# Kernel optimization log

Measured on AMD Instinct MI355X. Metric: run time of the kernel, lower is better.

The kernel has to match this reference:

```python
import jax, jax.numpy as jnp
import numpy as np

EPS = 1e-5
NH, NP = 4, 4  # num_heads, num_points (num_levels = 1)


def layer_norm(x, g, b):
    m = jnp.mean(x, -1, keepdims=True)
    xc = x - m
    v = jnp.mean(xc * xc, -1, keepdims=True)
    return xc * jax.lax.rsqrt(v + EPS) * g + b


def setup_inputs() -> dict:
    key = jax.random.key(0)
    ks = jax.random.split(key, 8)
    B, C, H, W = 8, 256, 64, 64
    s = 0.02
    return {
        "x1": jax.random.normal(ks[0], (B, C, H, W), jnp.float32),
        "x2": jax.random.normal(ks[1], (B, C, H, W), jnp.float32),
        "ln1_g": jnp.ones((C,), jnp.float32),
        "ln1_b": jnp.zeros((C,), jnp.float32),
        "ln2_g": jnp.ones((C,), jnp.float32),
        "ln2_b": jnp.zeros((C,), jnp.float32),
        "pos_scale": jnp.ones((1,), jnp.float32),
        "W_off": jax.random.normal(ks[2], (C, NH * NP * 2), jnp.float32) * s,
        "b_off": jax.random.normal(ks[3], (NH * NP * 2,), jnp.float32) * 0.5,
        "W_att": jax.random.normal(ks[4], (C, NH * NP), jnp.float32) * s,
        "b_att": jnp.zeros((NH * NP,), jnp.float32),
        "W_val": jax.random.normal(ks[5], (C, C), jnp.float32) * s,
        "b_val": jnp.zeros((C,), jnp.float32),
        "W_out": jax.random.normal(ks[6], (C, C), jnp.float32) * s,
        "b_out": jnp.zeros((C,), jnp.float32),
    }


def reference(x1, x2, ln1_g, ln1_b, ln2_g, ln2_b, pos_scale,
              W_off, b_off, W_att, b_att, W_val, b_val, W_out, b_out):
    B, C, H, W = x1.shape
    Nq = H * W
    d = C // NH
    q_in = x1.reshape(B, C, Nq).transpose(0, 2, 1)   # (B, Nq, C)
    v_in = x2.reshape(B, C, Nq).transpose(0, 2, 1)   # (B, Nv, C), identity

    # ScaledSinuEmbedding positional encoding over the query sequence
    inv_freq = 1.0 / (10000.0 ** (jnp.arange(0, C, 2, dtype=jnp.float32) / C))
    sinu = jnp.arange(Nq, dtype=jnp.float32)[:, None] * inv_freq[None, :]
    qpos = jnp.concatenate([jnp.sin(sinu), jnp.cos(sinu)], -1) * pos_scale  # (Nq, C)

    query = layer_norm(q_in, ln1_g, ln1_b) + qpos[None]
    value = layer_norm(v_in, ln2_g, ln2_b) @ W_val + b_val                 # (B, Nv, C)
    value = value.reshape(B, Nq, NH, d).transpose(0, 2, 1, 3)              # (B, NH, Nv, d)

    off = (query @ W_off + b_off).reshape(B, Nq, NH, NP, 2)
    att = jax.nn.softmax((query @ W_att + b_att).reshape(B, Nq, NH, NP), axis=-1)

    # reference points: normalized pixel centers of the query grid
    ry, rx = jnp.meshgrid((jnp.arange(H, dtype=jnp.float32) + 0.5) / H,
                          (jnp.arange(W, dtype=jnp.float32) + 0.5) / W,
                          indexing="ij")
    ref = jnp.stack([rx.ravel(), ry.ravel()], -1)                          # (Nq, 2) as (x, y)

    norm = jnp.array([W, H], jnp.float32)  # offset_normalizer = (W, H)
    loc = ref[None, :, None, None, :] + off / norm                         # (B,Nq,NH,NP,2)
    loc = loc.transpose(0, 2, 1, 3, 4)                                     # (B,NH,Nq,NP,2)
    # grid_sample(align_corners=False): pixel = normalized * size - 0.5
    px = loc[..., 0] * W - 0.5
    py = loc[..., 1] * H - 0.5
    x0 = jnp.floor(px); y0 = jnp.floor(py)
    wx = px - x0; wy = py - y0
    x0i = x0.astype(jnp.int32); y0i = y0.astype(jnp.int32)

    def gather(ix, iy):
        # zero padding for out-of-bounds corners, like grid_sample(padding_mode='zeros')
        valid = ((ix >= 0) & (ix < W) & (iy >= 0) & (iy < H)).astype(value.dtype)
        idx = jnp.clip(iy, 0, H - 1) * W + jnp.clip(ix, 0, W - 1)          # (B,NH,Nq,NP)
        g = jnp.take_along_axis(value, idx.reshape(B, NH, Nq * NP, 1), axis=2)
        return g.reshape(B, NH, Nq, NP, d) * valid[..., None]

    sampled = (gather(x0i, y0i) * ((1 - wx) * (1 - wy))[..., None]
               + gather(x0i + 1, y0i) * (wx * (1 - wy))[..., None]
               + gather(x0i, y0i + 1) * ((1 - wx) * wy)[..., None]
               + gather(x0i + 1, y0i + 1) * (wx * wy)[..., None])          # (B,NH,Nq,NP,d)

    out = jnp.sum(sampled * att.transpose(0, 2, 1, 3)[..., None], axis=3)  # (B,NH,Nq,d)
    out = out.transpose(0, 2, 1, 3).reshape(B, Nq, C)
    out = out @ W_out + b_out + v_in                                       # + identity (x2)
    return out.transpose(0, 2, 1).reshape(B, C, H, W)
```

## Files before the change

kernel.cpp:

```cpp
#include <hip/hip_runtime.h>
#include <math.h>

namespace {
constexpr int kC = 256;
constexpr int kNq = 4096;
constexpr int kM = 32768;
}

typedef __attribute__((ext_vector_type(8))) short short8;
typedef __attribute__((ext_vector_type(4))) short short4v;
typedef __attribute__((ext_vector_type(4))) float f32x4;

__device__ inline unsigned short f2bf(float f) {
  union { float f; unsigned u; } v; v.f = f;
  unsigned r = (v.u + 0x7FFFu + ((v.u >> 16) & 1u)) >> 16;
  return (unsigned short)r;
}
__device__ inline float bf2f(unsigned short h) {
  union { unsigned u; float f; } v; v.u = ((unsigned)h) << 16; return v.f;
}
__device__ inline float uasf(unsigned u) {
  union { unsigned u; float f; } v; v.u = u; return v.f;
}

__global__ __launch_bounds__(256)
void prep_weights_kernel(const float* __restrict__ Wv, const float* __restrict__ Wo,
                         const float* __restrict__ Woff, const float* __restrict__ Watt,
                         const float* __restrict__ boff, const float* __restrict__ batt,
                         const float* __restrict__ ps,
                         unsigned short* __restrict__ WvT, unsigned short* __restrict__ WoT,
                         unsigned short* __restrict__ WoaT, float* __restrict__ QP) {
  __shared__ unsigned short Aq[64][264];
  const int blk = blockIdx.x;
  const int tid = threadIdx.x;
  const int i = blk * 256 + tid;
  {
    const int n = i >> 8, k = i & 255;
    WvT[i] = f2bf(Wv[k * 256 + n]);
    WoT[i] = f2bf(Wo[k * 256 + n]);
  }
  if (i < 16384) {
    const int j = i >> 8, k = i & 255;
    float v = 0.f;
    if (j < 32) v = Woff[k * 32 + j];
    else if (j < 48) v = Watt[k * 16 + (j - 32)];
    WoaT[i] = f2bf(v);
  }
  if (blk >= 64) return;

  const float scale = ps[0];
  const int i2 = (tid < 128) ? tid : (tid - 128);
  const float invf = powf(10000.f, -(float)(2 * i2) * (1.f / 256.f));
  for (int q = 0; q < 64; ++q) {
    const float a = (float)(blk * 64 + q) * invf;
    Aq[q][tid] = f2bf(((tid < 128) ? sinf(a) : cosf(a)) * scale);
  }
  __syncthreads();

  const int lane = tid & 63, w = tid >> 6;
  const int l15 = lane & 15, quad = lane >> 4;
  f32x4 acc[3];
#pragma unroll
  for (int j = 0; j < 3; ++j) acc[j] = (f32x4){0.f, 0.f, 0.f, 0.f};
#pragma unroll
  for (int s = 0; s < 8; ++s) {
    short8 af = *(const short8*)&Aq[w * 16 + l15][s * 32 + quad * 8];
    short8 wf[3];
#pragma unroll
    for (int t = 0; t < 3; ++t)
#pragma unroll
      for (int j = 0; j < 8; ++j) {
        const int k = s * 32 + quad * 8 + j;
        wf[t][j] = (short)f2bf((t < 2) ? Woff[k * 32 + t * 16 + l15]
                                       : Watt[k * 16 + l15]);
      }
#pragma unroll
    for (int j = 0; j < 3; ++j)
      acc[j] = __builtin_amdgcn_mfma_f32_16x16x32_bf16(af, wf[j], acc[j], 0, 0, 0);
  }
#pragma unroll
  for (int j = 0; j < 3; ++j) {
    const int n = j * 16 + l15;
    const float bn = (n < 32) ? boff[n] : batt[n - 32];
#pragma unroll
    for (int r = 0; r < 4; ++r) {
      const int q = blk * 64 + w * 16 + quad * 4 + r;
      QP[q * 48 + n] = acc[j][r] + bn;
    }
  }
}

__global__ __launch_bounds__(256)
void fused_ln_gemm_kernel(const float* __restrict__ x1, const float* __restrict__ x2,
                          const float* __restrict__ ln1_g, const float* __restrict__ ln1_b,
                          const float* __restrict__ ln2_g, const float* __restrict__ ln2_b,
                          const unsigned short* __restrict__ WvT,
                          const float* __restrict__ b_val, unsigned short* __restrict__ V,
                          const unsigned short* __restrict__ WoaT,
                          const float* __restrict__ QP, float* __restrict__ RAW) {
  __shared__ unsigned short As[64][264];
  __shared__ unsigned short sx[256][36];
  __shared__ float psum[2][32][4];
  __shared__ float smean[64];
  __shared__ float srstd[64];

  const int mode = blockIdx.x & 1;
  const int m0 = (blockIdx.x >> 1) * 64;
  const int b = m0 >> 12;
  const int n0 = m0 & 4095;
  const int tid = threadIdx.x;
  const int lane = tid & 63, w = tid >> 6;
  const float gc = mode ? ln1_g[tid] : ln2_g[tid];
  const float bc = mode ? ln1_b[tid] : ln2_b[tid];
  const float* Xb = (mode ? x1 : x2) + (size_t)b * kC * kNq;

  const int cbase = tid >> 3;
  const int q4 = (tid & 7) * 4;
  float4 v[16];
#pragma unroll
  for (int g = 0; g < 2; ++g)
#pragma unroll
    for (int it = 0; it < 8; ++it)
      v[g * 8 + it] = *(const float4*)&Xb[(size_t)(it * 32 + cbase) * kNq + n0 + g * 32 + q4];

  for (int g = 0; g < 2; ++g) {
    float s[4] = {0.f, 0.f, 0.f, 0.f}, sq[4] = {0.f, 0.f, 0.f, 0.f};
#pragma unroll
    for (int it = 0; it < 8; ++it) {
      const float4 f4 = v[g * 8 + it];
      const float e[4] = {f4.x, f4.y, f4.z, f4.w};
      short4v pk;
#pragma unroll
      for (int j = 0; j < 4; ++j) {
        s[j] += e[j];
        sq[j] += e[j] * e[j];
        pk[j] = (short)f2bf(e[j]);
      }
      *(short4v*)&sx[it * 32 + cbase][q4] = pk;
    }
#pragma unroll
    for (int d = 8; d <= 32; d <<= 1)
#pragma unroll
      for (int j = 0; j < 4; ++j) {
        s[j] += __shfl_xor(s[j], d);
        sq[j] += __shfl_xor(sq[j], d);
      }
    if (lane < 8) {
#pragma unroll
      for (int j = 0; j < 4; ++j) {
        psum[0][lane * 4 + j][w] = s[j];
        psum[1][lane * 4 + j][w] = sq[j];
      }
    }
    __syncthreads();
    if (tid < 32) {
      float S = 0.f, Q = 0.f;
#pragma unroll
      for (int ww = 0; ww < 4; ++ww) { S += psum[0][tid][ww]; Q += psum[1][tid][ww]; }
      const float m = S * (1.f / 256.f);
      const float var = Q * (1.f / 256.f) - m * m;
      smean[g * 32 + tid] = m;
      srstd[g * 32 + tid] = rsqrtf(var + 1e-5f);
    }
    __syncthreads();
#pragma unroll
    for (int k = 0; k < 8; ++k) {
      const short4v xs = *(const short4v*)&sx[tid][k * 4];
#pragma unroll
      for (int j = 0; j < 4; ++j) {
        const int row = g * 32 + k * 4 + j;
        As[row][tid] = f2bf((bf2f((unsigned short)xs[j]) - smean[row]) * srstd[row] * gc + bc);
      }
    }
    __syncthreads();
  }

  const int l15 = lane & 15, quad = lane >> 4;

  if (mode == 0) {
    f32x4 acc[4][4];
#pragma unroll
    for (int i = 0; i < 4; ++i)
#pragma unroll
      for (int j = 0; j < 4; ++j) acc[i][j] = (f32x4){0.f, 0.f, 0.f, 0.f};
#pragma unroll
    for (int s = 0; s < 8; ++s) {
      short8 af[4], wf[4];
#pragma unroll
      for (int t = 0; t < 4; ++t) af[t] = *(const short8*)&As[t * 16 + l15][s * 32 + quad * 8];
#pragma unroll
      for (int t = 0; t < 4; ++t)
        wf[t] = *(const short8*)&WvT[(size_t)(w * 64 + t * 16 + l15) * 256 + s * 32 + quad * 8];
#pragma unroll
      for (int i = 0; i < 4; ++i)
#pragma unroll
        for (int j = 0; j < 4; ++j)
          acc[i][j] = __builtin_amdgcn_mfma_f32_16x16x32_bf16(af[i], wf[j], acc[i][j], 0, 0, 0);
    }
#pragma unroll
    for (int i = 0; i < 4; ++i)
#pragma unroll
      for (int j = 0; j < 4; ++j) {
        const int n = w * 64 + j * 16 + l15;
        const float bn = b_val[n];
#pragma unroll
        for (int r = 0; r < 4; ++r) {
          const int m = m0 + i * 16 + quad * 4 + r;
          V[(size_t)m * 256 + n] = f2bf(acc[i][j][r] + bn);
        }
      }
  } else {
    f32x4 acc[3];
#pragma unroll
    for (int j = 0; j < 3; ++j) acc[j] = (f32x4){0.f, 0.f, 0.f, 0.f};
#pragma unroll
    for (int s = 0; s < 8; ++s) {
      short8 af = *(const short8*)&As[w * 16 + l15][s * 32 + quad * 8];
      short8 wf[3];
#pragma unroll
      for (int t = 0; t < 3; ++t)
        wf[t] = *(const short8*)&WoaT[(size_t)(t * 16 + l15) * 256 + s * 32 + quad * 8];
#pragma unroll
      for (int j = 0; j < 3; ++j)
        acc[j] = __builtin_amdgcn_mfma_f32_16x16x32_bf16(af, wf[j], acc[j], 0, 0, 0);
    }
#pragma unroll
    for (int j = 0; j < 3; ++j) {
      const int n = j * 16 + l15;
#pragma unroll
      for (int r = 0; r < 4; ++r) {
        const int m = m0 + w * 16 + quad * 4 + r;
        const int q = n0 + w * 16 + quad * 4 + r;
        RAW[(size_t)m * 48 + n] = acc[j][r] + QP[q * 48 + n];
      }
    }
  }
}

__global__ __launch_bounds__(256)
void sample_out_kernel(const float* __restrict__ RAW, const unsigned short* __restrict__ V,
                       const unsigned short* __restrict__ Wt,
                       const float* __restrict__ bias, const float* __restrict__ x2,
                       float* __restrict__ OUT) {
  __shared__ unsigned short Bs[64][264];
  __shared__ __align__(16) char smemA[32768];
  int (*sidx)[4] = (int(*)[4])smemA;
  float (*swgt)[4] = (float(*)[4])(smemA + 16384);
  float* ot = (float*)smemA;

  const int blk = blockIdx.x;
  const int b = blk & 7;
  const int tile = blk >> 3;
  const int m0 = b * 4096 + tile * 64;
  const int tid = threadIdx.x;

#pragma unroll
  for (int t = 0; t < 4; ++t) {
    const int trip = t * 256 + tid;
    const int q_l = trip >> 4, h = (trip >> 2) & 3, p = trip & 3;
    const int m = m0 + q_l;
    const float* raw = RAW + (size_t)m * 48;
    const float l0 = raw[32 + h * 4 + 0];
    const float l1 = raw[32 + h * 4 + 1];
    const float l2 = raw[32 + h * 4 + 2];
    const float l3 = raw[32 + h * 4 + 3];
    const float mx = fmaxf(fmaxf(l0, l1), fmaxf(l2, l3));
    const float e0 = expf(l0 - mx), e1 = expf(l1 - mx), e2 = expf(l2 - mx), e3 = expf(l3 - mx);
    const float lp = (p == 0) ? e0 : (p == 1) ? e1 : (p == 2) ? e2 : e3;
    const float attp = lp / (e0 + e1 + e2 + e3);

    const float ox = raw[h * 8 + p * 2 + 0];
    const float oy = raw[h * 8 + p * 2 + 1];
    const float px = (float)(m & 63) + ox;
    const float py = (float)((m >> 6) & 63) + oy;
    const float fx = floorf(px), fy = floorf(py);
    const float wx = px - fx, wy = py - fy;
    const int x0 = (int)fx, y0 = (int)fy;
#pragma unroll
    for (int c = 0; c < 4; ++c) {
      const int dx = c & 1, dy = c >> 1;
      const int xx = x0 + dx, yy = y0 + dy;
      const bool valid = (xx >= 0) & (xx < 64) & (yy >= 0) & (yy < 64);
      const float wc = (dx ? wx : 1.f - wx) * (dy ? wy : 1.f - wy) * attp;
      swgt[trip][c] = valid ? wc : 0.f;
      const int xc = min(max(xx, 0), 63), yc = min(max(yy, 0), 63);
      sidx[trip][c] = yc * 64 + xc;
    }
  }
  __syncthreads();

#pragma unroll
  for (int it = 0; it < 8; ++it) {
    const int lin = it * 256 + tid;
    const int q_l = lin >> 5, sub = lin & 31;
    const int h = sub >> 3, c8 = (sub & 7) * 8;
    const int trip0 = q_l * 16 + h * 4;
    const unsigned short* vb = V + (size_t)b * kNq * kC + h * 64 + c8;
    float acc[8] = {};
#pragma unroll
    for (int p = 0; p < 4; ++p) {
      const int4 idx = *(const int4*)&sidx[trip0 + p][0];
      const float4 wv = *(const float4*)&swgt[trip0 + p][0];
      const int ia[4] = {idx.x, idx.y, idx.z, idx.w};
      const float wa[4] = {wv.x, wv.y, wv.z, wv.w};
#pragma unroll
      for (int c = 0; c < 4; ++c) {
        const uint4 u = *(const uint4*)&vb[(size_t)ia[c] * kC];
        const float w = wa[c];
        acc[0] = fmaf(w, uasf(u.x << 16), acc[0]);
        acc[1] = fmaf(w, uasf(u.x & 0xffff0000u), acc[1]);
        acc[2] = fmaf(w, uasf(u.y << 16), acc[2]);
        acc[3] = fmaf(w, uasf(u.y & 0xffff0000u), acc[3]);
        acc[4] = fmaf(w, uasf(u.z << 16), acc[4]);
        acc[5] = fmaf(w, uasf(u.z & 0xffff0000u), acc[5]);
        acc[6] = fmaf(w, uasf(u.w << 16), acc[6]);
        acc[7] = fmaf(w, uasf(u.w & 0xffff0000u), acc[7]);
      }
    }
    short8 outv;
#pragma unroll
    for (int e = 0; e < 8; ++e) outv[e] = (short)f2bf(acc[e]);
    *(short8*)&Bs[q_l][h * 64 + c8] = outv;
  }
  __syncthreads();

  const int lane = tid & 63, w = tid >> 6;
  const int l15 = lane & 15, quad = lane >> 4;
  f32x4 acc[4][4];
#pragma unroll
  for (int i = 0; i < 4; ++i)
#pragma unroll
    for (int j = 0; j < 4; ++j) acc[i][j] = (f32x4){0.f, 0.f, 0.f, 0.f};
#pragma unroll
  for (int s = 0; s < 8; ++s) {
    short8 wf[4], bf[4];
#pragma unroll
    for (int t = 0; t < 4; ++t)
      wf[t] = *(const short8*)&Wt[(size_t)(w * 64 + t * 16 + l15) * 256 + s * 32 + quad * 8];
#pragma unroll
    for (int t = 0; t < 4; ++t) bf[t] = *(const short8*)&Bs[t * 16 + l15][s * 32 + quad * 8];
#pragma unroll
    for (int i = 0; i < 4; ++i)
#pragma unroll
      for (int j = 0; j < 4; ++j)
        acc[i][j] = __builtin_amdgcn_mfma_f32_16x16x32_bf16(wf[i], bf[j], acc[i][j], 0, 0, 0);
  }

  const int whalf = w >> 1;
  const int clbase = (w & 1) * 64;
  for (int ch = 0; ch < 2; ++ch) {
    __syncthreads();
    if (whalf == ch) {
#pragma unroll
      for (int i = 0; i < 4; ++i)
#pragma unroll
        for (int j = 0; j < 4; ++j)
#pragma unroll
          for (int r = 0; r < 4; ++r)
            ot[(clbase + i * 16 + quad * 4 + r) * 64 + j * 16 + l15] = acc[i][j][r];
    }
    __syncthreads();
#pragma unroll
    for (int t = 0; t < 8; ++t) {
      const int lin = t * 256 + tid;
      const int cl = lin >> 4, q4 = (lin & 15) * 4;
      const int c = ch * 128 + cl;
      const size_t rowbase = ((size_t)b * 256 + c) * 4096 + tile * 64;
      const float4 xv = *(const float4*)&x2[rowbase + q4];
      const float bc = bias[c];
      float4 o;
      o.x = ot[cl * 64 + q4 + 0] + bc + xv.x;
      o.y = ot[cl * 64 + q4 + 1] + bc + xv.y;
      o.z = ot[cl * 64 + q4 + 2] + bc + xv.z;
      o.w = ot[cl * 64 + q4 + 3] + bc + xv.w;
      *(float4*)&OUT[rowbase + q4] = o;
    }
  }
}

extern "C" void kernel_launch(void* const* d_in, const int* in_sizes, int n_in,
                              void* d_out, int out_size, void* d_ws, size_t ws_size,
                              hipStream_t stream) {
  const float* x1 = (const float*)d_in[0];
  const float* x2 = (const float*)d_in[1];
  const float* ln1_g = (const float*)d_in[2];
  const float* ln1_b = (const float*)d_in[3];
  const float* ln2_g = (const float*)d_in[4];
  const float* ln2_b = (const float*)d_in[5];
  const float* pos_scale = (const float*)d_in[6];
  const float* W_off = (const float*)d_in[7];
  const float* b_off = (const float*)d_in[8];
  const float* W_att = (const float*)d_in[9];
  const float* b_att = (const float*)d_in[10];
  const float* W_val = (const float*)d_in[11];
  const float* b_val = (const float*)d_in[12];
  const float* W_out = (const float*)d_in[13];
  const float* b_out = (const float*)d_in[14];
  float* out = (float*)d_out;

  char* ws = (char*)d_ws;
  const size_t plane2 = (size_t)kM * kC * sizeof(unsigned short);
  unsigned short* Vb   = (unsigned short*)(ws);
  float* RAW           = (float*)(ws + plane2);
  unsigned short* WvT  = (unsigned short*)(ws + plane2 + (size_t)kM * 48 * 4);
  unsigned short* WoT  = WvT + 65536;
  unsigned short* WoaT = WoT + 65536;
  float* QP            = (float*)(WoaT + 16384);

  prep_weights_kernel<<<256, 256, 0, stream>>>(W_val, W_out, W_off, W_att,
                                               b_off, b_att, pos_scale,
                                               WvT, WoT, WoaT, QP);
  fused_ln_gemm_kernel<<<1024, 256, 0, stream>>>(x1, x2, ln1_g, ln1_b, ln2_g, ln2_b,
                                                 WvT, b_val, Vb, WoaT, QP, RAW);
  sample_out_kernel<<<512, 256, 0, stream>>>(RAW, Vb, WoT, b_out, x2, out);
}
```

Baseline: 192.5 us.

## Restructure LN load mapping to drop staging buffer and spread positional prep

The fused LayerNorm+GEMM kernel now has each thread load 8 consecutive channels. It computes mean and variance for both 32-row groups in one pass and writes the normalized bf16 rows straight into the GEMM tile. This removes the bf16 staging buffer sx, two barriers per group, and a bf16 round-trip of x, and raises occupancy through launch bounds. The positional-encoding projection in prep_weights is spread over all blocks at 16 queries each, using angle-addition recurrences instead of per-element sin/cos. The recurrence can accumulate small rounding drift, and the new global load pattern is less coalesced per channel row.

```diff
diff --git a/kernel.cpp b/kernel.cpp
--- a/kernel.cpp
+++ b/kernel.cpp
@@ -15,9 +15,6 @@
   union { float f; unsigned u; } v; v.f = f;
   unsigned r = (v.u + 0x7FFFu + ((v.u >> 16) & 1u)) >> 16;
   return (unsigned short)r;
-}
-__device__ inline float bf2f(unsigned short h) {
-  union { unsigned u; float f; } v; v.u = ((unsigned)h) << 16; return v.f;
 }
 __device__ inline float uasf(unsigned u) {
   union { unsigned u; float f; } v; v.u = u; return v.f;
@@ -30,7 +27,7 @@
                          const float* __restrict__ ps,
                          unsigned short* __restrict__ WvT, unsigned short* __restrict__ WoT,
                          unsigned short* __restrict__ WoaT, float* __restrict__ QP) {
-  __shared__ unsigned short Aq[64][264];
+  __shared__ unsigned short Aq[16][264];
   const int blk = blockIdx.x;
   const int tid = threadIdx.x;
   const int i = blk * 256 + tid;
@@ -46,51 +43,50 @@
     else if (j < 48) v = Watt[k * 16 + (j - 32)];
     WoaT[i] = f2bf(v);
   }
-  if (blk >= 64) return;
 
   const float scale = ps[0];
   const int i2 = (tid < 128) ? tid : (tid - 128);
   const float invf = powf(10000.f, -(float)(2 * i2) * (1.f / 256.f));
-  for (int q = 0; q < 64; ++q) {
-    const float a = (float)(blk * 64 + q) * invf;
-    Aq[q][tid] = f2bf(((tid < 128) ? sinf(a) : cosf(a)) * scale);
+  const int q0 = blk * 16;
+  const float a0 = (float)q0 * invf;
+  float sv = sinf(a0), cv = cosf(a0);
+  const float sd = sinf(invf), cd = cosf(invf);
+#pragma unroll
+  for (int q = 0; q < 16; ++q) {
+    Aq[q][tid] = f2bf(((tid < 128) ? sv : cv) * scale);
+    const float ns = sv * cd + cv * sd;
+    const float nc = cv * cd - sv * sd;
+    sv = ns; cv = nc;
   }
   __syncthreads();
 
   const int lane = tid & 63, w = tid >> 6;
   const int l15 = lane & 15, quad = lane >> 4;
-  f32x4 acc[3];
-#pragma unroll
-  for (int j = 0; j < 3; ++j) acc[j] = (f32x4){0.f, 0.f, 0.f, 0.f};
-#pragma unroll
-  for (int s = 0; s < 8; ++s) {
-    short8 af = *(const short8*)&Aq[w * 16 + l15][s * 32 + quad * 8];
-    short8 wf[3];
-#pragma unroll
-    for (int t = 0; t < 3; ++t)
+  if (w < 3) {
+    f32x4 acc = (f32x4){0.f, 0.f, 0.f, 0.f};
+#pragma unroll
+    for (int s = 0; s < 8; ++s) {
+      const short8 af = *(const short8*)&Aq[l15][s * 32 + quad * 8];
+      short8 wf;
 #pragma unroll
       for (int j = 0; j < 8; ++j) {
         const int k = s * 32 + quad * 8 + j;
-        wf[t][j] = (short)f2bf((t < 2) ? Woff[k * 32 + t * 16 + l15]
-                                       : Watt[k * 16 + l15]);
-      }
-#pragma unroll
-    for (int j = 0; j < 3; ++j)
-      acc[j] = __builtin_amdgcn_mfma_f32_16x16x32_bf16(af, wf[j], acc[j], 0, 0, 0);
-  }
-#pragma unroll
-  for (int j = 0; j < 3; ++j) {
-    const int n = j * 16 + l15;
+        wf[j] = (short)f2bf((w < 2) ? Woff[k * 32 + w * 16 + l15]
+                                    : Watt[k * 16 + l15]);
+      }
+      acc = __builtin_amdgcn_mfma_f32_16x16x32_bf16(af, wf, acc, 0, 0, 0);
+    }
+    const int n = w * 16 + l15;
     const float bn = (n < 32) ? boff[n] : batt[n - 32];
 #pragma unroll
     for (int r = 0; r < 4; ++r) {
-      const int q = blk * 64 + w * 16 + quad * 4 + r;
-      QP[q * 48 + n] = acc[j][r] + bn;
-    }
-  }
-}
-
-__global__ __launch_bounds__(256)
+      const int q = q0 + quad * 4 + r;
+      QP[q * 48 + n] = acc[r] + bn;
+    }
+  }
+}
+
+__global__ __launch_bounds__(256, 4)
 void fused_ln_gemm_kernel(const float* __restrict__ x1, const float* __restrict__ x2,
                           const float* __restrict__ ln1_g, const float* __restrict__ ln1_b,
                           const float* __restrict__ ln2_g, const float* __restrict__ ln2_b,
@@ -99,8 +95,8 @@
                           const unsigned short* __restrict__ WoaT,
                           const float* __restrict__ QP, float* __restrict__ RAW) {
   __shared__ unsigned short As[64][264];
-  __shared__ unsigned short sx[256][36];
   __shared__ float psum[2][32][4];
+  __shared__ float psq[2][32][4];
   __shared__ float smean[64];
   __shared__ float srstd[64];
 
@@ -110,70 +106,91 @@
   const int n0 = m0 & 4095;
   const int tid = threadIdx.x;
   const int lane = tid & 63, w = tid >> 6;
-  const float gc = mode ? ln1_g[tid] : ln2_g[tid];
-  const float bc = mode ? ln1_b[tid] : ln2_b[tid];
+  const int l7 = tid & 7;
+  const int q4 = l7 * 4;
+  const int cb8 = (tid >> 3) * 8;
   const float* Xb = (mode ? x1 : x2) + (size_t)b * kC * kNq;
-
-  const int cbase = tid >> 3;
-  const int q4 = (tid & 7) * 4;
+  const float* gptr = mode ? ln1_g : ln2_g;
+  const float* bptr = mode ? ln1_b : ln2_b;
+
+  float4 gm[2], bv[2];
+  gm[0] = *(const float4*)&gptr[cb8];
+  gm[1] = *(const float4*)&gptr[cb8 + 4];
+  bv[0] = *(const float4*)&bptr[cb8];
+  bv[1] = *(const float4*)&bptr[cb8 + 4];
+
   float4 v[16];
 #pragma unroll
   for (int g = 0; g < 2; ++g)
 #pragma unroll
     for (int it = 0; it < 8; ++it)
-      v[g * 8 + it] = *(const float4*)&Xb[(size_t)(it * 32 + cbase) * kNq + n0 + g * 32 + q4];
-
+      v[g * 8 + it] = *(const float4*)&Xb[(size_t)(cb8 + it) * kNq + n0 + g * 32 + q4];
+
+  float s[2][4] = {}, sq[2][4] = {};
+#pragma unroll
+  for (int g = 0; g < 2; ++g)
+#pragma unroll
+    for (int it = 0; it < 8; ++it) {
+      const float* e = (const float*)&v[g * 8 + it];
+#pragma unroll
+      for (int j = 0; j < 4; ++j) {
+        s[g][j] += e[j];
+        sq[g][j] += e[j] * e[j];
+      }
+    }
+#pragma unroll
+  for (int d = 8; d <= 32; d <<= 1)
+#pragma unroll
+    for (int g = 0; g < 2; ++g)
+#pragma unroll
+      for (int j = 0; j < 4; ++j) {
+        s[g][j] += __shfl_xor(s[g][j], d);
+        sq[g][j] += __shfl_xor(sq[g][j], d);
+      }
+  if (lane < 8) {
+#pragma unroll
+    for (int g = 0; g < 2; ++g)
+#pragma unroll
+      for (int j = 0; j < 4; ++j) {
+        psum[g][q4 + j][w] = s[g][j];
+        psq[g][q4 + j][w] = sq[g][j];
+      }
+  }
+  __syncthreads();
+  if (tid < 64) {
+    const int g = tid >> 5, qq = tid & 31;
+    float S = 0.f, Q = 0.f;
+#pragma unroll
+    for (int ww = 0; ww < 4; ++ww) { S += psum[g][qq][ww]; Q += psq[g][qq][ww]; }
+    const float m = S * (1.f / 256.f);
+    const float var = Q * (1.f / 256.f) - m * m;
+    smean[tid] = m;
+    srstd[tid] = rsqrtf(var + 1e-5f);
+  }
+  __syncthreads();
+
+#pragma unroll
   for (int g = 0; g < 2; ++g) {
-    float s[4] = {0.f, 0.f, 0.f, 0.f}, sq[4] = {0.f, 0.f, 0.f, 0.f};
-#pragma unroll
-    for (int it = 0; it < 8; ++it) {
-      const float4 f4 = v[g * 8 + it];
-      const float e[4] = {f4.x, f4.y, f4.z, f4.w};
-      short4v pk;
-#pragma unroll
-      for (int j = 0; j < 4; ++j) {
-        s[j] += e[j];
-        sq[j] += e[j] * e[j];
-        pk[j] = (short)f2bf(e[j]);
-      }
-      *(short4v*)&sx[it * 32 + cbase][q4] = pk;
-    }
-#pragma unroll
-    for (int d = 8; d <= 32; d <<= 1)
-#pragma unroll
-      for (int j = 0; j < 4; ++j) {
-        s[j] += __shfl_xor(s[j], d);
-        sq[j] += __shfl_xor(sq[j], d);
-      }
-    if (lane < 8) {
-#pragma unroll
-      for (int j = 0; j < 4; ++j) {
-        psum[0][lane * 4 + j][w] = s[j];
-        psum[1][lane * 4 + j][w] = sq[j];
-      }
-    }
-    __syncthreads();
-    if (tid < 32) {
-      float S = 0.f, Q = 0.f;
-#pragma unroll
-      for (int ww = 0; ww < 4; ++ww) { S += psum[0][tid][ww]; Q += psum[1][tid][ww]; }
-      const float m = S * (1.f / 256.f);
-      const float var = Q * (1.f / 256.f) - m * m;
-      smean[g * 32 + tid] = m;
-      srstd[g * 32 + tid] = rsqrtf(var + 1e-5f);
-    }
-    __syncthreads();
-#pragma unroll
-    for (int k = 0; k < 8; ++k) {
-      const short4v xs = *(const short4v*)&sx[tid][k * 4];
-#pragma unroll
-      for (int j = 0; j < 4; ++j) {
-        const int row = g * 32 + k * 4 + j;
-        As[row][tid] = f2bf((bf2f((unsigned short)xs[j]) - smean[row]) * srstd[row] * gc + bc);
-      }
-    }
-    __syncthreads();
-  }
+    const float4 mn = *(const float4*)&smean[g * 32 + q4];
+    const float4 rs = *(const float4*)&srstd[g * 32 + q4];
+    const float* mnp = (const float*)&mn;
+    const float* rsp = (const float*)&rs;
+#pragma unroll
+    for (int j = 0; j < 4; ++j) {
+      const int row = g * 32 + q4 + j;
+      short4v pk0, pk1;
+#pragma unroll
+      for (int it = 0; it < 4; ++it) {
+        const float e0 = ((const float*)&v[g * 8 + it])[j];
+        const float e1 = ((const float*)&v[g * 8 + 4 + it])[j];
+        pk0[it] = (short)f2bf((e0 - mnp[j]) * rsp[j] * ((const float*)gm)[it] + ((const float*)bv)[it]);
+        pk1[it] = (short)f2bf((e1 - mnp[j]) * rsp[j] * ((const float*)gm)[4 + it] + ((const float*)bv)[4 + it]);
+      }
+      *(short4v*)&As[row][cb8] = pk0;
+      *(short4v*)&As[row][cb8 + 4] = pk1;
+    }
+  }
+  __syncthreads();
 
   const int l15 = lane & 15, quad = lane >> 4;
 
@@ -184,13 +201,13 @@
 #pragma unroll
       for (int j = 0; j < 4; ++j) acc[i][j] = (f32x4){0.f, 0.f, 0.f, 0.f};
 #pragma unroll
-    for (int s = 0; s < 8; ++s) {
+    for (int s2 = 0; s2 < 8; ++s2) {
       short8 af[4], wf[4];
 #pragma unroll
-      for (int t = 0; t < 4; ++t) af[t] = *(const short8*)&As[t * 16 + l15][s * 32 + quad * 8];
+      for (int t = 0; t < 4; ++t) af[t] = *(const short8*)&As[t * 16 + l15][s2 * 32 + quad * 8];
 #pragma unroll
       for (int t = 0; t < 4; ++t)
-        wf[t] = *(const short8*)&WvT[(size_t)(w * 64 + t * 16 + l15) * 256 + s * 32 + quad * 8];
+        wf[t] = *(const short8*)&WvT[(size_t)(w * 64 + t * 16 + l15) * 256 + s2 * 32 + quad * 8];
 #pragma unroll
       for (int i = 0; i < 4; ++i)
 #pragma unroll
@@ -214,12 +231,12 @@
 #pragma unroll
     for (int j = 0; j < 3; ++j) acc[j] = (f32x4){0.f, 0.f, 0.f, 0.f};
 #pragma unroll
-    for (int s = 0; s < 8; ++s) {
-      short8 af = *(const short8*)&As[w * 16 + l15][s * 32 + quad * 8];
+    for (int s2 = 0; s2 < 8; ++s2) {
+      short8 af = *(const short8*)&As[w * 16 + l15][s2 * 32 + quad * 8];
       short8 wf[3];
 #pragma unroll
       for (int t = 0; t < 3; ++t)
-        wf[t] = *(const short8*)&WoaT[(size_t)(t * 16 + l15) * 256 + s * 32 + quad * 8];
+        wf[t] = *(const short8*)&WoaT[(size_t)(t * 16 + l15) * 256 + s2 * 32 + quad * 8];
 #pragma unroll
       for (int j = 0; j < 3; ++j)
         acc[j] = __builtin_amdgcn_mfma_f32_16x16x32_bf16(af, wf[j], acc[j], 0, 0, 0);
```

Result: faster. 174.9 us (-9.1%).
